# Performance work log

Measured on AMD Instinct MI355X. Metric: run time of the kernel, lower is better.

The kernel has to match this reference:

```python
import jax, jax.numpy as jnp
import numpy as np

E = 1024      # embed_dim
H = 16        # num_heads
D = E // H    # head_dim
SCALING = float(D * 1.0) ** (-0.5)


def setup_inputs() -> dict:
    key = jax.random.key(0)
    ks = jax.random.split(key, 10)
    B, L, S = 4, 2048, 2048
    query = jax.random.normal(ks[0], (B, L, E), dtype=jnp.float32)
    k_in = jax.random.normal(ks[1], (B, S, E), dtype=jnp.float32)
    v_in = jax.random.normal(ks[2], (B, S, E), dtype=jnp.float32)
    attn_bias = jax.random.normal(ks[3], (L, S), dtype=jnp.float32)
    attn_mask = jax.random.normal(ks[4], (L, S), dtype=jnp.float32)
    # in_proj: Linear(E, 3E)  (xavier-uniform-ish scale), out_proj: Linear(E, E)
    lim_in = np.sqrt(6.0 / (E + 3 * E))
    Wqkv = jax.random.uniform(ks[5], (3 * E, E), minval=-lim_in, maxval=lim_in, dtype=jnp.float32)
    bqkv = jnp.zeros((3 * E,), dtype=jnp.float32)
    lim_out = np.sqrt(1.0 / E)
    Wo = jax.random.uniform(ks[6], (E, E), minval=-lim_out, maxval=lim_out, dtype=jnp.float32)
    bo = jnp.zeros((E,), dtype=jnp.float32)
    return {"query": query, "key": k_in, "value": v_in,
            "attn_bias": attn_bias, "attn_mask": attn_mask,
            "Wqkv": Wqkv, "bqkv": bqkv, "Wo": Wo, "bo": bo}


def reference(query, key, value, attn_bias, attn_mask, Wqkv, bqkv, Wo, bo):
    B, L, _ = query.shape
    S = key.shape[1]
    # fused in_proj split into q/k/v slices (q from query, k from key, v from value)
    q = query @ Wqkv[:E].T + bqkv[:E]
    k = key @ Wqkv[E:2 * E].T + bqkv[E:2 * E]
    v = value @ Wqkv[2 * E:].T + bqkv[2 * E:]
    q = q * SCALING
    # [B, L, H, D]
    q = q.reshape(B, L, H, D)
    k = k.reshape(B, S, H, D)
    v = v.reshape(B, S, H, D)
    # scores: [B, H, L, S] with additive float mask and bias (broadcast over B, H)
    scores = jnp.einsum("blhd,bshd->bhls", q, k)
    scores = scores + attn_mask[None, None] + attn_bias[None, None]
    weights = jax.nn.softmax(scores, axis=-1)  # dropout p=0.0 -> identity
    out = jnp.einsum("bhls,bshd->blhd", weights, v).reshape(B, L, E)
    return out @ Wo.T + bo
```

## Files before the change

kernel.cpp:

```cpp
#include <hip/hip_runtime.h>
#include <hip/hip_bf16.h>

#define BB 4
#define LL 2048
#define SS 2048
#define EE 1024
#define HH 16
#define DD 64
#define MM (BB * LL)

typedef unsigned short u16;
typedef u16   u16x4  __attribute__((ext_vector_type(4)));
typedef u16   u16x8  __attribute__((ext_vector_type(8)));
typedef float f32x4  __attribute__((ext_vector_type(4)));
typedef __bf16 bf16x8 __attribute__((ext_vector_type(8)));

__device__ __forceinline__ u16 f2bf(float x) {
    unsigned u = __float_as_uint(x);
    u += 0x7fffu + ((u >> 16) & 1u);
    return (u16)(u >> 16);
}
__device__ __forceinline__ float bf2f(u16 b) {
    return __uint_as_float(((unsigned)b) << 16);
}

__global__ __launch_bounds__(256) void f32_to_bf16_kernel(
    const float* __restrict__ in, u16* __restrict__ out)
{
    size_t idx = ((size_t)blockIdx.x * 256 + threadIdx.x) * 8;
    f32x4 a = *(const f32x4*)(in + idx);
    f32x4 b = *(const f32x4*)(in + idx + 4);
    u16x8 o;
#pragma unroll
    for (int j = 0; j < 4; j++) { o[j] = f2bf(a[j]); o[4 + j] = f2bf(b[j]); }
    *(u16x8*)(out + idx) = o;
}

__global__ __launch_bounds__(256) void combine_bias_kernel(
    const float* __restrict__ bias, const float* __restrict__ mask,
    u16* __restrict__ comb)
{
    int idx = (blockIdx.x * 256 + threadIdx.x) * 8;
    f32x4 a0 = *(const f32x4*)(bias + idx);
    f32x4 a1 = *(const f32x4*)(bias + idx + 4);
    f32x4 m0 = *(const f32x4*)(mask + idx);
    f32x4 m1 = *(const f32x4*)(mask + idx + 4);
    u16x8 o;
#pragma unroll
    for (int j = 0; j < 4; j++) { o[j] = f2bf(a0[j] + m0[j]); o[4 + j] = f2bf(a1[j] + m1[j]); }
    *(u16x8*)(comb + idx) = o;
}

template <int ABF16, int OUTBF16>
__global__ __launch_bounds__(256, 2) void gemm_bt(
    const void* __restrict__ Ap, const u16* __restrict__ Bw,
    const float* __restrict__ bias, void* __restrict__ Cp,
    int M, int N, int K, float scale)
{
    __shared__ __align__(16) u16 As[128 * 72];
    __shared__ __align__(16) u16 Bs[128 * 72];
    const int tid = threadIdx.x;
    const int lane = tid & 63, wave = tid >> 6;
    const int quad = lane >> 4, ln = lane & 15;
    const int wm = (wave & 1) * 64, wn = (wave >> 1) * 64;
    const int m0 = blockIdx.x * 128, n0 = blockIdx.y * 128;

    f32x4 acc[4][4];
#pragma unroll
    for (int mt = 0; mt < 4; mt++)
#pragma unroll
        for (int nt = 0; nt < 4; nt++) acc[mt][nt] = (f32x4){0.f, 0.f, 0.f, 0.f};

    const float* Af = (const float*)Ap;
    const u16*   Ab = (const u16*)Ap;

    f32x4 apf[8];
    u16x8 apb[4];
    u16x8 bpf[4];

    auto load_tiles = [&](int k0) {
        if (ABF16) {
#pragma unroll
            for (int i = 0; i < 4; i++) {
                int chunk = tid + 256 * i, row = chunk >> 3, c = chunk & 7;
                apb[i] = *(const u16x8*)(Ab + (size_t)(m0 + row) * K + k0 + c * 8);
            }
        } else {
#pragma unroll
            for (int i = 0; i < 8; i++) {
                int chunk = tid + 256 * i, row = chunk >> 4, c = chunk & 15;
                apf[i] = *(const f32x4*)(Af + (size_t)(m0 + row) * K + k0 + c * 4);
            }
        }
#pragma unroll
        for (int i = 0; i < 4; i++) {
            int chunk = tid + 256 * i, row = chunk >> 3, c = chunk & 7;
            bpf[i] = *(const u16x8*)(Bw + (size_t)(n0 + row) * K + k0 + c * 8);
        }
    };

    load_tiles(0);

    for (int k0 = 0; k0 < K; k0 += 64) {
        __syncthreads();
        if (ABF16) {
#pragma unroll
            for (int i = 0; i < 4; i++) {
                int chunk = tid + 256 * i, row = chunk >> 3, c = chunk & 7;
                *(u16x8*)(As + row * 72 + c * 8) = apb[i];
            }
        } else {
#pragma unroll
            for (int i = 0; i < 8; i++) {
                int chunk = tid + 256 * i, row = chunk >> 4, c = chunk & 15;
                u16x4 o;
#pragma unroll
                for (int j = 0; j < 4; j++) o[j] = f2bf(apf[i][j]);
                *(u16x4*)(As + row * 72 + c * 4) = o;
            }
        }
#pragma unroll
        for (int i = 0; i < 4; i++) {
            int chunk = tid + 256 * i, row = chunk >> 3, c = chunk & 7;
            *(u16x8*)(Bs + row * 72 + c * 8) = bpf[i];
        }
        __syncthreads();

        if (k0 + 64 < K) load_tiles(k0 + 64);

#pragma unroll
        for (int ks = 0; ks < 2; ks++) {
            bf16x8 af[4], bfg[4];
#pragma unroll
            for (int mt = 0; mt < 4; mt++)
                af[mt] = *(const bf16x8*)(As + (wm + mt * 16 + ln) * 72 + ks * 32 + quad * 8);
#pragma unroll
            for (int nt = 0; nt < 4; nt++)
                bfg[nt] = *(const bf16x8*)(Bs + (wn + nt * 16 + ln) * 72 + ks * 32 + quad * 8);
#pragma unroll
            for (int mt = 0; mt < 4; mt++)
#pragma unroll
                for (int nt = 0; nt < 4; nt++)
                    acc[mt][nt] = __builtin_amdgcn_mfma_f32_16x16x32_bf16(
                        af[mt], bfg[nt], acc[mt][nt], 0, 0, 0);
        }
    }

#pragma unroll
    for (int nt = 0; nt < 4; nt++) {
        int n = n0 + wn + nt * 16 + ln;
        float bn = bias[n];
#pragma unroll
        for (int mt = 0; mt < 4; mt++) {
#pragma unroll
            for (int r = 0; r < 4; r++) {
                int m = m0 + wm + mt * 16 + quad * 4 + r;
                float val = (acc[mt][nt][r] + bn) * scale;
                if (OUTBF16) ((u16*)Cp)[(size_t)m * N + n] = f2bf(val);
                else         ((float*)Cp)[(size_t)m * N + n] = val;
            }
        }
    }
}

__global__ __launch_bounds__(256) void transpose_v_kernel(
    const u16* __restrict__ vb, u16* __restrict__ vt)
{
    __shared__ __align__(16) u16 t[64 * 72];
    const int bh = blockIdx.y, b = bh >> 4, h = bh & 15;
    const int s0 = blockIdx.x * 64;
    const int tid = threadIdx.x;
#pragma unroll
    for (int i = 0; i < 2; i++) {
        int chunk = tid + 256 * i;
        int row = chunk >> 3, c = chunk & 7;
        u16x8 v = *(const u16x8*)(vb + (size_t)(b * SS + s0 + row) * EE + h * 64 + c * 8);
        *(u16x8*)(t + row * 72 + c * 8) = v;
    }
    __syncthreads();
#pragma unroll
    for (int i = 0; i < 2; i++) {
        int chunk = tid + 256 * i;
        int d = chunk >> 3, c = chunk & 7;
        u16x8 o;
#pragma unroll
        for (int j = 0; j < 8; j++) o[j] = t[(c * 8 + j) * 72 + d];
        *(u16x8*)(vt + (size_t)(bh * 64 + d) * SS + s0 + c * 8) = o;
    }
}

__global__ __launch_bounds__(256, 2) void attn_kernel(
    const u16* __restrict__ qb,
    const u16* __restrict__ kb,
    const u16* __restrict__ vt,
    const u16* __restrict__ comb,
    u16* __restrict__ attn)
{
    __shared__ __align__(16) u16 KPs[128 * 136];
    __shared__ __align__(16) u16 Vs[64 * 136];
    const int tid = threadIdx.x, lane = tid & 63, wave = tid >> 6;
    const int quad = lane >> 4, ln = lane & 15;
    const int bh = blockIdx.y, b = bh >> 4, h = bh & 15;
    const int q0 = blockIdx.x * 128;
    const int qloc0 = wave * 32;

    bf16x8 qf[2][2];
#pragma unroll
    for (int qg = 0; qg < 2; qg++)
#pragma unroll
        for (int ks = 0; ks < 2; ks++)
            qf[qg][ks] = *(const bf16x8*)(qb + (size_t)(b * LL + q0 + qloc0 + 16 * qg + ln) * EE
                                          + h * 64 + ks * 32 + quad * 8);

    const u16* cb0 = comb + (size_t)(q0 + qloc0 + ln) * SS + quad * 4;
    const u16* cb1 = cb0 + (size_t)16 * SS;

    f32x4 o[4][2];
#pragma unroll
    for (int mt = 0; mt < 4; mt++) { o[mt][0] = (f32x4){0,0,0,0}; o[mt][1] = (f32x4){0,0,0,0}; }
    float lsum0 = 0.f, lsum1 = 0.f;

    u16x8 kreg[4], vreg[4];
    auto load_kv = [&](int s0) {
#pragma unroll
        for (int i = 0; i < 4; i++) {
            int chunk = tid + 256 * i, row = chunk >> 3, c = chunk & 7;
            kreg[i] = *(const u16x8*)(kb + (size_t)(b * SS + s0 + row) * EE + h * 64 + c * 8);
        }
#pragma unroll
        for (int i = 0; i < 4; i++) {
            int chunk = tid + 256 * i, row = chunk >> 4, c = chunk & 15;
            vreg[i] = *(const u16x8*)(vt + (size_t)(bh * 64 + row) * SS + s0 + c * 8);
        }
    };
    load_kv(0);

    for (int s0 = 0; s0 < SS; s0 += 128) {
        __syncthreads();
#pragma unroll
        for (int i = 0; i < 4; i++) {
            int chunk = tid + 256 * i, row = chunk >> 3, c = chunk & 7;
            *(u16x8*)(KPs + row * 72 + c * 8) = kreg[i];
        }
#pragma unroll
        for (int i = 0; i < 4; i++) {
            int chunk = tid + 256 * i, row = chunk >> 4, c = chunk & 15;
            *(u16x8*)(Vs + row * 136 + c * 8) = vreg[i];
        }
        __syncthreads();

        if (s0 + 128 < SS) load_kv(s0 + 128);

        u16x4 bfr[8][2];
#pragma unroll
        for (int mt = 0; mt < 8; mt++) {
            bfr[mt][0] = *(const u16x4*)(cb0 + s0 + mt * 16);
            bfr[mt][1] = *(const u16x4*)(cb1 + s0 + mt * 16);
        }

        f32x4 st[8][2];
#pragma unroll
        for (int mt = 0; mt < 8; mt++) {
            bf16x8 a0 = *(const bf16x8*)(KPs + (mt * 16 + ln) * 72 + quad * 8);
            bf16x8 a1 = *(const bf16x8*)(KPs + (mt * 16 + ln) * 72 + 32 + quad * 8);
#pragma unroll
            for (int qg = 0; qg < 2; qg++) {
                f32x4 z = (f32x4){0,0,0,0};
                z = __builtin_amdgcn_mfma_f32_16x16x32_bf16(a0, qf[qg][0], z, 0, 0, 0);
                z = __builtin_amdgcn_mfma_f32_16x16x32_bf16(a1, qf[qg][1], z, 0, 0, 0);
                st[mt][qg] = z;
            }
        }

        u16x4 p[8][2];
#pragma unroll
        for (int mt = 0; mt < 8; mt++)
#pragma unroll
            for (int qg = 0; qg < 2; qg++) {
#pragma unroll
                for (int r = 0; r < 4; r++) {
                    float e = __expf(st[mt][qg][r] + bf2f(bfr[mt][qg][r]));
                    if (qg == 0) lsum0 += e; else lsum1 += e;
                    p[mt][qg][r] = f2bf(e);
                }
            }

        __syncthreads();

#pragma unroll
        for (int mt = 0; mt < 8; mt++) {
            *(u16x4*)(KPs + (qloc0 + ln) * 136 + mt * 16 + quad * 4)      = p[mt][0];
            *(u16x4*)(KPs + (qloc0 + 16 + ln) * 136 + mt * 16 + quad * 4) = p[mt][1];
        }

#pragma unroll
        for (int ks = 0; ks < 4; ks++) {
            bf16x8 pf0 = *(const bf16x8*)(KPs + (qloc0 + ln) * 136 + ks * 32 + quad * 8);
            bf16x8 pf1 = *(const bf16x8*)(KPs + (qloc0 + 16 + ln) * 136 + ks * 32 + quad * 8);
#pragma unroll
            for (int mt = 0; mt < 4; mt++) {
                bf16x8 a = *(const bf16x8*)(Vs + (mt * 16 + ln) * 136 + ks * 32 + quad * 8);
                o[mt][0] = __builtin_amdgcn_mfma_f32_16x16x32_bf16(a, pf0, o[mt][0], 0, 0, 0);
                o[mt][1] = __builtin_amdgcn_mfma_f32_16x16x32_bf16(a, pf1, o[mt][1], 0, 0, 0);
            }
        }
    }

    lsum0 += __shfl_xor(lsum0, 16); lsum0 += __shfl_xor(lsum0, 32);
    lsum1 += __shfl_xor(lsum1, 16); lsum1 += __shfl_xor(lsum1, 32);
    float inv0 = 1.f / lsum0, inv1 = 1.f / lsum1;

#pragma unroll
    for (int mt = 0; mt < 4; mt++) {
        u16x4 p0, p1;
#pragma unroll
        for (int r = 0; r < 4; r++) { p0[r] = f2bf(o[mt][0][r] * inv0); p1[r] = f2bf(o[mt][1][r] * inv1); }
        *(u16x4*)(KPs + (qloc0 + ln) * 136 + mt * 16 + quad * 4)      = p0;
        *(u16x4*)(KPs + (qloc0 + 16 + ln) * 136 + mt * 16 + quad * 4) = p1;
    }
#pragma unroll
    for (int i = 0; i < 4; i++) {
        int j = lane + 64 * i;
        int r = j >> 3, c = j & 7;
        u16x8 v = *(const u16x8*)(KPs + (qloc0 + r) * 136 + c * 8);
        *(u16x8*)(attn + (size_t)(b * LL + q0 + qloc0 + r) * EE + h * 64 + c * 8) = v;
    }
}

extern "C" void kernel_launch(void* const* d_in, const int* in_sizes, int n_in,
                              void* d_out, int out_size, void* d_ws, size_t ws_size,
                              hipStream_t stream)
{
    (void)in_sizes; (void)n_in; (void)out_size; (void)ws_size;
    const float* query     = (const float*)d_in[0];
    const float* key       = (const float*)d_in[1];
    const float* value     = (const float*)d_in[2];
    const float* attn_bias = (const float*)d_in[3];
    const float* attn_mask = (const float*)d_in[4];
    const float* Wqkv      = (const float*)d_in[5];
    const float* bqkv      = (const float*)d_in[6];
    const float* Wo        = (const float*)d_in[7];
    const float* bo        = (const float*)d_in[8];
    float* out = (float*)d_out;

    u16* wq_bf = (u16*)d_ws;
    u16* wo_bf = wq_bf + 3 * EE * EE;
    u16* comb  = wo_bf + EE * EE;
    u16* q_bf  = comb + (size_t)LL * SS;
    u16* k_bf  = q_bf + (size_t)MM * EE;
    u16* v_bf  = k_bf + (size_t)MM * EE;
    u16* vtr   = v_bf + (size_t)MM * EE;
    u16* attnb = vtr  + (size_t)MM * EE;

    f32_to_bf16_kernel<<<3 * EE * EE / 2048, 256, 0, stream>>>(Wqkv, wq_bf);
    f32_to_bf16_kernel<<<EE * EE / 2048, 256, 0, stream>>>(Wo, wo_bf);
    combine_bias_kernel<<<(LL * SS) / 2048, 256, 0, stream>>>(attn_bias, attn_mask, comb);

    dim3 gg(MM / 128, EE / 128);
    gemm_bt<0, 1><<<gg, 256, 0, stream>>>(query, wq_bf,               bqkv,          q_bf, MM, EE, EE, 0.125f);
    gemm_bt<0, 1><<<gg, 256, 0, stream>>>(key,   wq_bf + EE * EE,     bqkv + EE,     k_bf, MM, EE, EE, 1.f);
    gemm_bt<0, 1><<<gg, 256, 0, stream>>>(value, wq_bf + 2 * EE * EE, bqkv + 2 * EE, v_bf, MM, EE, EE, 1.f);

    transpose_v_kernel<<<dim3(SS / 64, BB * HH), 256, 0, stream>>>(v_bf, vtr);

    attn_kernel<<<dim3(LL / 128, BB * HH), 256, 0, stream>>>(q_bf, k_bf, vtr, comb, attnb);

    gemm_bt<1, 0><<<gg, 256, 0, stream>>>(attnb, wo_bf, bo, out, MM, EE, EE, 1.f);
}
```

Before: 444.5 us.

## Use async LDS loads in GEMM, exp2 softmax with folded log2e, prio hints

The GEMM is rebuilt around double-buffered LDS tiles filled with global_load_lds, dropping register staging and the fused fp32 conversion. The fp32 activations are now converted to bf16 by separate passes before each projection. In attention, log2e is folded into the Q scale and the combined bias so softmax uses exp2. The bias is also loaded straight into the score accumulator, row sums go into vector accumulators, occupancy is raised to 3 blocks, and setprio hints are placed around the MFMA sections. The change aims to hide global-load latency and trim softmax ALU work, but adds extra conversion passes over the inputs. The unpadded 64-wide LDS rows may also cause bank conflicts.

```diff
diff --git a/kernel.cpp b/kernel.cpp
--- a/kernel.cpp
+++ b/kernel.cpp
@@ -8,11 +8,13 @@
 #define HH 16
 #define DD 64
 #define MM (BB * LL)
+#define LOG2E 1.44269504088896340736f
 
 typedef unsigned short u16;
 typedef u16   u16x4  __attribute__((ext_vector_type(4)));
 typedef u16   u16x8  __attribute__((ext_vector_type(8)));
 typedef float f32x4  __attribute__((ext_vector_type(4)));
+typedef __bf16 bf16x4 __attribute__((ext_vector_type(4)));
 typedef __bf16 bf16x8 __attribute__((ext_vector_type(8)));
 
 __device__ __forceinline__ u16 f2bf(float x) {
@@ -22,6 +24,12 @@
 }
 __device__ __forceinline__ float bf2f(u16 b) {
     return __uint_as_float(((unsigned)b) << 16);
+}
+
+__device__ __forceinline__ void gload16(const u16* g, u16* l) {
+    __builtin_amdgcn_global_load_lds(
+        (const __attribute__((address_space(1))) void*)g,
+        (__attribute__((address_space(3))) void*)l, 16, 0, 0);
 }
 
 __global__ __launch_bounds__(256) void f32_to_bf16_kernel(
@@ -47,96 +55,63 @@
     f32x4 m1 = *(const f32x4*)(mask + idx + 4);
     u16x8 o;
 #pragma unroll
-    for (int j = 0; j < 4; j++) { o[j] = f2bf(a0[j] + m0[j]); o[4 + j] = f2bf(a1[j] + m1[j]); }
+    for (int j = 0; j < 4; j++) {
+        o[j]     = f2bf((a0[j] + m0[j]) * LOG2E);
+        o[4 + j] = f2bf((a1[j] + m1[j]) * LOG2E);
+    }
     *(u16x8*)(comb + idx) = o;
 }
 
-template <int ABF16, int OUTBF16>
-__global__ __launch_bounds__(256, 2) void gemm_bt(
-    const void* __restrict__ Ap, const u16* __restrict__ Bw,
+template <int OUTBF16>
+__global__ __launch_bounds__(256, 2) void gemm_bt_bf16(
+    const u16* __restrict__ A, const u16* __restrict__ Bw,
     const float* __restrict__ bias, void* __restrict__ Cp,
     int M, int N, int K, float scale)
 {
-    __shared__ __align__(16) u16 As[128 * 72];
-    __shared__ __align__(16) u16 Bs[128 * 72];
+    __shared__ __align__(16) u16 As[2][128 * 64];
+    __shared__ __align__(16) u16 Bs[2][128 * 64];
     const int tid = threadIdx.x;
     const int lane = tid & 63, wave = tid >> 6;
     const int quad = lane >> 4, ln = lane & 15;
     const int wm = (wave & 1) * 64, wn = (wave >> 1) * 64;
     const int m0 = blockIdx.x * 128, n0 = blockIdx.y * 128;
 
+    const int r8 = lane >> 3, c8 = lane & 7;
+    const u16* Ag = A  + (size_t)m0 * K + c8 * 8;
+    const u16* Bg = Bw + (size_t)n0 * K + c8 * 8;
+
     f32x4 acc[4][4];
 #pragma unroll
     for (int mt = 0; mt < 4; mt++)
 #pragma unroll
         for (int nt = 0; nt < 4; nt++) acc[mt][nt] = (f32x4){0.f, 0.f, 0.f, 0.f};
 
-    const float* Af = (const float*)Ap;
-    const u16*   Ab = (const u16*)Ap;
-
-    f32x4 apf[8];
-    u16x8 apb[4];
-    u16x8 bpf[4];
-
-    auto load_tiles = [&](int k0) {
-        if (ABF16) {
-#pragma unroll
-            for (int i = 0; i < 4; i++) {
-                int chunk = tid + 256 * i, row = chunk >> 3, c = chunk & 7;
-                apb[i] = *(const u16x8*)(Ab + (size_t)(m0 + row) * K + k0 + c * 8);
-            }
-        } else {
-#pragma unroll
-            for (int i = 0; i < 8; i++) {
-                int chunk = tid + 256 * i, row = chunk >> 4, c = chunk & 15;
-                apf[i] = *(const f32x4*)(Af + (size_t)(m0 + row) * K + k0 + c * 4);
-            }
-        }
-#pragma unroll
-        for (int i = 0; i < 4; i++) {
-            int chunk = tid + 256 * i, row = chunk >> 3, c = chunk & 7;
-            bpf[i] = *(const u16x8*)(Bw + (size_t)(n0 + row) * K + k0 + c * 8);
+    auto stage = [&](int buf, int k0) {
+#pragma unroll
+        for (int i = 0; i < 4; i++) {
+            int ch = i * 4 + wave;
+            int row = ch * 8 + r8;
+            gload16(Ag + (size_t)row * K + k0, &As[buf][ch * 512]);
+            gload16(Bg + (size_t)row * K + k0, &Bs[buf][ch * 512]);
         }
     };
 
-    load_tiles(0);
-
-    for (int k0 = 0; k0 < K; k0 += 64) {
+    stage(0, 0);
+    int buf = 0;
+    const int KT = K >> 6;
+    for (int kt = 0; kt < KT; kt++) {
         __syncthreads();
-        if (ABF16) {
-#pragma unroll
-            for (int i = 0; i < 4; i++) {
-                int chunk = tid + 256 * i, row = chunk >> 3, c = chunk & 7;
-                *(u16x8*)(As + row * 72 + c * 8) = apb[i];
-            }
-        } else {
-#pragma unroll
-            for (int i = 0; i < 8; i++) {
-                int chunk = tid + 256 * i, row = chunk >> 4, c = chunk & 15;
-                u16x4 o;
-#pragma unroll
-                for (int j = 0; j < 4; j++) o[j] = f2bf(apf[i][j]);
-                *(u16x4*)(As + row * 72 + c * 4) = o;
-            }
-        }
-#pragma unroll
-        for (int i = 0; i < 4; i++) {
-            int chunk = tid + 256 * i, row = chunk >> 3, c = chunk & 7;
-            *(u16x8*)(Bs + row * 72 + c * 8) = bpf[i];
-        }
-        __syncthreads();
-
-        if (k0 + 64 < K) load_tiles(k0 + 64);
-
+        if (kt + 1 < KT) stage(buf ^ 1, (kt + 1) << 6);
+        __builtin_amdgcn_s_setprio(1);
 #pragma unroll
         for (int ks = 0; ks < 2; ks++) {
             bf16x8 af[4], bfg[4];
 #pragma unroll
             for (int mt = 0; mt < 4; mt++)
-                af[mt] = *(const bf16x8*)(As + (wm + mt * 16 + ln) * 72 + ks * 32 + quad * 8);
+                af[mt] = *(const bf16x8*)(&As[buf][(wm + mt * 16 + ln) * 64 + ks * 32 + quad * 8]);
 #pragma unroll
             for (int nt = 0; nt < 4; nt++)
-                bfg[nt] = *(const bf16x8*)(Bs + (wn + nt * 16 + ln) * 72 + ks * 32 + quad * 8);
+                bfg[nt] = *(const bf16x8*)(&Bs[buf][(wn + nt * 16 + ln) * 64 + ks * 32 + quad * 8]);
 #pragma unroll
             for (int mt = 0; mt < 4; mt++)
 #pragma unroll
@@ -144,6 +119,8 @@
                     acc[mt][nt] = __builtin_amdgcn_mfma_f32_16x16x32_bf16(
                         af[mt], bfg[nt], acc[mt][nt], 0, 0, 0);
         }
+        __builtin_amdgcn_s_setprio(0);
+        buf ^= 1;
     }
 
 #pragma unroll
@@ -189,7 +166,7 @@
     }
 }
 
-__global__ __launch_bounds__(256, 2) void attn_kernel(
+__global__ __launch_bounds__(256, 3) void attn_kernel(
     const u16* __restrict__ qb,
     const u16* __restrict__ kb,
     const u16* __restrict__ vt,
@@ -218,7 +195,7 @@
     f32x4 o[4][2];
 #pragma unroll
     for (int mt = 0; mt < 4; mt++) { o[mt][0] = (f32x4){0,0,0,0}; o[mt][1] = (f32x4){0,0,0,0}; }
-    float lsum0 = 0.f, lsum1 = 0.f;
+    f32x4 ls0 = (f32x4){0,0,0,0}, ls1 = (f32x4){0,0,0,0};
 
     u16x8 kreg[4], vreg[4];
     auto load_kv = [&](int s0) {
@@ -247,76 +224,88 @@
             int chunk = tid + 256 * i, row = chunk >> 4, c = chunk & 15;
             *(u16x8*)(Vs + row * 136 + c * 8) = vreg[i];
         }
-        __syncthreads();
-
-        if (s0 + 128 < SS) load_kv(s0 + 128);
-
         u16x4 bfr[8][2];
 #pragma unroll
         for (int mt = 0; mt < 8; mt++) {
             bfr[mt][0] = *(const u16x4*)(cb0 + s0 + mt * 16);
             bfr[mt][1] = *(const u16x4*)(cb1 + s0 + mt * 16);
         }
+        __syncthreads();
+
+        if (s0 + 128 < SS) load_kv(s0 + 128);
 
         f32x4 st[8][2];
+#pragma unroll
+        for (int mt = 0; mt < 8; mt++)
+#pragma unroll
+            for (int r = 0; r < 4; r++) {
+                st[mt][0][r] = bf2f(bfr[mt][0][r]);
+                st[mt][1][r] = bf2f(bfr[mt][1][r]);
+            }
+
+        __builtin_amdgcn_s_setprio(1);
 #pragma unroll
         for (int mt = 0; mt < 8; mt++) {
             bf16x8 a0 = *(const bf16x8*)(KPs + (mt * 16 + ln) * 72 + quad * 8);
             bf16x8 a1 = *(const bf16x8*)(KPs + (mt * 16 + ln) * 72 + 32 + quad * 8);
-#pragma unroll
-            for (int qg = 0; qg < 2; qg++) {
-                f32x4 z = (f32x4){0,0,0,0};
-                z = __builtin_amdgcn_mfma_f32_16x16x32_bf16(a0, qf[qg][0], z, 0, 0, 0);
-                z = __builtin_amdgcn_mfma_f32_16x16x32_bf16(a1, qf[qg][1], z, 0, 0, 0);
-                st[mt][qg] = z;
+            st[mt][0] = __builtin_amdgcn_mfma_f32_16x16x32_bf16(a0, qf[0][0], st[mt][0], 0, 0, 0);
+            st[mt][0] = __builtin_amdgcn_mfma_f32_16x16x32_bf16(a1, qf[0][1], st[mt][0], 0, 0, 0);
+            st[mt][1] = __builtin_amdgcn_mfma_f32_16x16x32_bf16(a0, qf[1][0], st[mt][1], 0, 0, 0);
+            st[mt][1] = __builtin_amdgcn_mfma_f32_16x16x32_bf16(a1, qf[1][1], st[mt][1], 0, 0, 0);
+        }
+        __builtin_amdgcn_s_setprio(0);
+
+        bf16x4 p[8][2];
+#pragma unroll
+        for (int mt = 0; mt < 8; mt++)
+#pragma unroll
+            for (int r = 0; r < 4; r++) {
+                float e0 = __builtin_amdgcn_exp2f(st[mt][0][r]);
+                float e1 = __builtin_amdgcn_exp2f(st[mt][1][r]);
+                ls0[r] += e0; ls1[r] += e1;
+                p[mt][0][r] = (__bf16)e0;
+                p[mt][1][r] = (__bf16)e1;
             }
-        }
-
-        u16x4 p[8][2];
-#pragma unroll
-        for (int mt = 0; mt < 8; mt++)
-#pragma unroll
-            for (int qg = 0; qg < 2; qg++) {
-#pragma unroll
-                for (int r = 0; r < 4; r++) {
-                    float e = __expf(st[mt][qg][r] + bf2f(bfr[mt][qg][r]));
-                    if (qg == 0) lsum0 += e; else lsum1 += e;
-                    p[mt][qg][r] = f2bf(e);
-                }
-            }
 
         __syncthreads();
 
 #pragma unroll
         for (int mt = 0; mt < 8; mt++) {
-            *(u16x4*)(KPs + (qloc0 + ln) * 136 + mt * 16 + quad * 4)      = p[mt][0];
-            *(u16x4*)(KPs + (qloc0 + 16 + ln) * 136 + mt * 16 + quad * 4) = p[mt][1];
+            *(bf16x4*)(KPs + (qloc0 + ln) * 136 + mt * 16 + quad * 4)      = p[mt][0];
+            *(bf16x4*)(KPs + (qloc0 + 16 + ln) * 136 + mt * 16 + quad * 4) = p[mt][1];
         }
 
 #pragma unroll
         for (int ks = 0; ks < 4; ks++) {
             bf16x8 pf0 = *(const bf16x8*)(KPs + (qloc0 + ln) * 136 + ks * 32 + quad * 8);
             bf16x8 pf1 = *(const bf16x8*)(KPs + (qloc0 + 16 + ln) * 136 + ks * 32 + quad * 8);
+            __builtin_amdgcn_s_setprio(1);
 #pragma unroll
             for (int mt = 0; mt < 4; mt++) {
                 bf16x8 a = *(const bf16x8*)(Vs + (mt * 16 + ln) * 136 + ks * 32 + quad * 8);
                 o[mt][0] = __builtin_amdgcn_mfma_f32_16x16x32_bf16(a, pf0, o[mt][0], 0, 0, 0);
                 o[mt][1] = __builtin_amdgcn_mfma_f32_16x16x32_bf16(a, pf1, o[mt][1], 0, 0, 0);
             }
-        }
-    }
-
+            __builtin_amdgcn_s_setprio(0);
+        }
+    }
+
+    float lsum0 = (ls0[0] + ls0[1]) + (ls0[2] + ls0[3]);
+    float lsum1 = (ls1[0] + ls1[1]) + (ls1[2] + ls1[3]);
     lsum0 += __shfl_xor(lsum0, 16); lsum0 += __shfl_xor(lsum0, 32);
     lsum1 += __shfl_xor(lsum1, 16); lsum1 += __shfl_xor(lsum1, 32);
     float inv0 = 1.f / lsum0, inv1 = 1.f / lsum1;
 
 #pragma unroll
     for (int mt = 0; mt < 4; mt++) {
-        u16x4 p0, p1;
-#pragma unroll
-        for (int r = 0; r < 4; r++) { p0[r] = f2bf(o[mt][0][r] * inv0); p1[r] = f2bf(o[mt][1][r] * inv1); }
-        *(u16x4*)(KPs + (qloc0 + ln) * 136 + mt * 16 + quad * 4)      = p0;
-        *(u16x4*)(KPs + (qloc0 + 16 + ln) * 136 + mt * 16 + quad * 4) = p1;
+        bf16x4 p0, p1;
+#pragma unroll
+        for (int r = 0; r < 4; r++) {
+            p0[r] = (__bf16)(o[mt][0][r] * inv0);
+            p1[r] = (__bf16)(o[mt][1][r] * inv1);
+        }
+        *(bf16x4*)(KPs + (qloc0 + ln) * 136 + mt * 16 + quad * 4)      = p0;
+        *(bf16x4*)(KPs + (qloc0 + 16 + ln) * 136 + mt * 16 + quad * 4) = p1;
     }
 #pragma unroll
     for (int i = 0; i < 4; i++) {
@@ -351,19 +340,23 @@
     u16* v_bf  = k_bf + (size_t)MM * EE;
     u16* vtr   = v_bf + (size_t)MM * EE;
     u16* attnb = vtr  + (size_t)MM * EE;
+    u16* tmp   = attnb;
 
     f32_to_bf16_kernel<<<3 * EE * EE / 2048, 256, 0, stream>>>(Wqkv, wq_bf);
     f32_to_bf16_kernel<<<EE * EE / 2048, 256, 0, stream>>>(Wo, wo_bf);
     combine_bias_kernel<<<(LL * SS) / 2048, 256, 0, stream>>>(attn_bias, attn_mask, comb);
 
     dim3 gg(MM / 128, EE / 128);
-    gemm_bt<0, 1><<<gg, 256, 0, stream>>>(query, wq_bf,               bqkv,          q_bf, MM, EE, EE, 0.125f);
-    gemm_bt<0, 1><<<gg, 256, 0, stream>>>(key,   wq_bf + EE * EE,     bqkv + EE,     k_bf, MM, EE, EE, 1.f);
-    gemm_bt<0, 1><<<gg, 256, 0, stream>>>(value, wq_bf + 2 * EE * EE, bqkv + 2 * EE, v_bf, MM, EE, EE, 1.f);
+    f32_to_bf16_kernel<<<(int)((size_t)MM * EE / 2048), 256, 0, stream>>>(query, tmp);
+    gemm_bt_bf16<1><<<gg, 256, 0, stream>>>(tmp, wq_bf,              bqkv,          q_bf, MM, EE, EE, 0.125f * LOG2E);
+    f32_to_bf16_kernel<<<(int)((size_t)MM * EE / 2048), 256, 0, stream>>>(key, tmp);
+    gemm_bt_bf16<1><<<gg, 256, 0, stream>>>(tmp, wq_bf + EE * EE,     bqkv + EE,     k_bf, MM, EE, EE, 1.f);
+    f32_to_bf16_kernel<<<(int)((size_t)MM * EE / 2048), 256, 0, stream>>>(value, tmp);
+    gemm_bt_bf16<1><<<gg, 256, 0, stream>>>(tmp, wq_bf + 2 * EE * EE, bqkv + 2 * EE, v_bf, MM, EE, EE, 1.f);
 
     transpose_v_kernel<<<dim3(SS / 64, BB * HH), 256, 0, stream>>>(v_bf, vtr);
 
     attn_kernel<<<dim3(LL / 128, BB * HH), 256, 0, stream>>>(q_bf, k_bf, vtr, comb, attnb);
 
-    gemm_bt<1, 0><<<gg, 256, 0, stream>>>(attnb, wo_bf, bo, out, MM, EE, EE, 1.f);
-}
+    gemm_bt_bf16<0><<<gg, 256, 0, stream>>>(attnb, wo_bf, bo, out, MM, EE, EE, 1.f);
+}
```

Result: slower. 556.5 us (+25.2%).
